# Optimization experiments

Hardware: AMD Instinct MI355X
Metric: run time of the kernel (lower is better)

The kernel has to match this reference:

```python
import jax, jax.numpy as jnp
import numpy as np

B, T, V, D = 4, 2048, 1024, 512


def setup_inputs() -> dict:
    key = jax.random.key(0)
    ks = jax.random.split(key, 6)
    x = jax.random.normal(ks[0], (B, T, V), dtype=jnp.float32)
    decay_logit = jax.random.uniform(ks[1], (), dtype=jnp.float32)
    scale = jnp.ones((), dtype=jnp.float32)
    std = 0.02
    # Linear weights stored as [in, out] so projection is x @ W
    Wq = std * jax.random.normal(ks[2], (V, D), dtype=jnp.float32)
    Wk = std * jax.random.normal(ks[3], (V, D), dtype=jnp.float32)
    Wv = std * jax.random.normal(ks[4], (V, D), dtype=jnp.float32)
    Wo = std * jax.random.normal(ks[5], (D, V), dtype=jnp.float32)
    return {"x": x, "decay_logit": decay_logit, "scale": scale,
            "Wq": Wq, "Wk": Wk, "Wv": Wv, "Wo": Wo}


def reference(x, decay_logit, scale, Wq, Wk, Wv, Wo):
    dtype = x.dtype
    xf = x.astype(jnp.float32)
    q = (xf @ Wq).astype(dtype)  # [B,T,D]
    k = (xf @ Wk).astype(dtype)
    v = (xf @ Wv).astype(dtype)
    scores = jnp.einsum('btd,bsd->bts', q, k)  # [B,T,T]
    decay = jax.nn.sigmoid(decay_logit)
    pos = jnp.arange(T)
    diff = pos[None, :] - pos[:, None]  # diff[i,j] = j - i
    expo = jnp.maximum(diff.astype(jnp.float32) - 1.0, 0.0)
    weights = (decay ** expo) * (diff > 0)  # [T,T]
    scores = scores * weights.astype(dtype)[None, :, :]
    retrieved = jnp.einsum('bts,bsd->btd', scores, v)  # [B,T,D]
    out = (retrieved.astype(jnp.float32) @ Wo).astype(dtype) * scale
    return out
```

## Files before the change

kernel.cpp:

```cpp
#include <hip/hip_runtime.h>
#include <stdint.h>


using bf16u = unsigned short;
using short8 = __attribute__((ext_vector_type(8))) short;
using f32x4  = __attribute__((ext_vector_type(4))) float;

__device__ __forceinline__ unsigned short f2bf(float f) {
  unsigned int u = __float_as_uint(f);
  u += 0x7fffu + ((u >> 16) & 1u);
  return (unsigned short)(u >> 16);
}

__device__ __forceinline__ void gload16(const void* g, void* l) {
  __builtin_amdgcn_global_load_lds(
      (const __attribute__((address_space(1))) void*)g,
      (__attribute__((address_space(3))) void*)l, 16, 0, 0);
}

#define BM 128
#define BN 128
#define BK 32

template<int MODE>
__global__ __launch_bounds__(256)
void gemm_bt(const bf16u* __restrict__ A, const bf16u* __restrict__ Bt,
             void* __restrict__ Cout,
             int K, int ldA, int ldB, int ldC,
             long sA, long sB, long sC,
             int nbx, const float* __restrict__ scal,
             const bf16u* __restrict__ vSrc, bf16u* __restrict__ vDst)
{
  __shared__ bf16u Al[2][BM * BK];
  __shared__ bf16u Bl[2][BN * BK];
  const int z = blockIdx.z;
  A  += (long)z * sA;
  Bt += (long)z * sB;

  const int tid  = threadIdx.x;
  const int orig = blockIdx.x;

  int by, bx;
  if (MODE == 1) {
    if (orig >= 32) {
      const int ti = orig - 32;
      const int c0 = (ti & 15) * 32;
      const int r0 = (ti >> 4) * 32;
      bf16u* tl = (bf16u*)&Al[0][0];
      const int tx = tid & 31, ty = tid >> 5;
      const bf16u* vin = vSrc + (long)z * (2048L * 1536);
      bf16u*      vout = vDst + (long)z * (1L << 20);
#pragma unroll
      for (int i = 0; i < 4; ++i)
        tl[(ty + 8 * i) * 33 + tx] = vin[(long)(r0 + ty + 8 * i) * 1536 + c0 + tx];
      __syncthreads();
#pragma unroll
      for (int i = 0; i < 4; ++i)
        vout[(long)(c0 + ty + 8 * i) * 2048 + r0 + tx] = tl[tx * 33 + ty + 8 * i];
      return;
    }
    by = orig >> 1; bx = orig & 1;
  } else {
    const int nwg = gridDim.x;
    const int q8 = nwg >> 3, r8 = nwg & 7;
    const int xcd = orig & 7, lid = orig >> 3;
    const int wgid = (xcd < r8 ? xcd * (q8 + 1)
                               : r8 * (q8 + 1) + (xcd - r8) * q8) + lid;
    by = wgid / nbx; bx = wgid - by * nbx;
  }
  const int bm = by * BM;
  const int bn = (MODE == 1) ? ((bm >> 7) + bx) * BN : bx * BN;
  const int kofsB = (MODE == 3) ? (bm & ~127) : 0;

  const int wid  = tid >> 6;
  const int lane = tid & 63;
  const int wr = (wid >> 1) * 64;
  const int wc = (wid & 1) * 64;

  f32x4 acc[4][4] = {};

  const int base0 = wid * 1024;
  const int lin0  = base0 + lane * 16;
  const int r0row = lin0 >> 6;
  const int r1row = r0row + 64;
  const int c16   = (lin0 >> 4) & 3;
  const int rcol  = (c16 ^ ((r0row >> 1) & 3)) << 3;

  const int nt = K / BK;

  auto stage = [&](int buf, int kk) {
    gload16(A  + (long)(bm + r0row) * ldA + kk + rcol, (char*)&Al[buf][0] + base0);
    gload16(A  + (long)(bm + r1row) * ldA + kk + rcol, (char*)&Al[buf][0] + base0 + 4096);
    gload16(Bt + (long)(bn + r0row) * ldB + kofsB + kk + rcol, (char*)&Bl[buf][0] + base0);
    gload16(Bt + (long)(bn + r1row) * ldB + kofsB + kk + rcol, (char*)&Bl[buf][0] + base0 + 4096);
  };

  stage(0, 0);
  __syncthreads();

  const int fr = lane & 15;
  const int kc = lane >> 4;
  int cur = 0;
  for (int t = 0; t < nt; ++t) {
    if (t + 1 < nt) stage(cur ^ 1, (t + 1) * BK);
    short8 af[4], bfr[4];
#pragma unroll
    for (int m = 0; m < 4; ++m) {
      int row = wr + m * 16 + fr;
      af[m] = *(const short8*)&Al[cur][row * BK + ((kc ^ ((row >> 1) & 3)) << 3)];
    }
#pragma unroll
    for (int n = 0; n < 4; ++n) {
      int row = wc + n * 16 + fr;
      bfr[n] = *(const short8*)&Bl[cur][row * BK + ((kc ^ ((row >> 1) & 3)) << 3)];
    }
#pragma unroll
    for (int m = 0; m < 4; ++m)
#pragma unroll
      for (int n = 0; n < 4; ++n)
        acc[m][n] = __builtin_amdgcn_mfma_f32_16x16x32_bf16(af[m], bfr[n], acc[m][n], 0, 0, 0);
    __syncthreads();
    cur ^= 1;
  }

  const int cc = lane & 15;
  const int cr = (lane >> 4) * 4;
  float mul = 1.0f, l2d = 0.0f;
  if (MODE == 1) {
    float dlv = scal[0];
    float decay = 1.0f / (1.0f + __expf(-dlv));
    l2d = __log2f(decay);
  } else if (MODE == 2) {
    mul = scal[0];
  }

#pragma unroll
  for (int m = 0; m < 4; ++m) {
#pragma unroll
    for (int n = 0; n < 4; ++n) {
#pragma unroll
      for (int j = 0; j < 4; ++j) {
        int row = bm + wr + m * 16 + cr + j;
        int col = bn + wc + n * 16 + cc;
        float val = acc[m][n][j];
        if (MODE == 1) {
          int diff = col - row;
          float w = (diff > 0 && col < 2048)
                        ? exp2f((float)(diff - 1) * l2d) : 0.0f;
          int lc = bx * 128 + (wc + n * 16 + cc);
          ((bf16u*)Cout)[(long)z * sC + (long)row * ldC + lc] = f2bf(val * w);
        } else if (MODE == 2) {
          ((float*)Cout)[(long)z * sC + (long)row * ldC + col] = val * mul;
        } else {
          ((bf16u*)Cout)[(long)z * sC + (long)row * ldC + col] = f2bf(val);
        }
      }
    }
  }
}

__global__ __launch_bounds__(256)
void prep(const float4* __restrict__ x, ushort4* __restrict__ x16o,
          const float* __restrict__ Wq, const float* __restrict__ Wk,
          const float* __restrict__ Wv, const float* __restrict__ Wo,
          bf16u* __restrict__ WqT, bf16u* __restrict__ WkT,
          bf16u* __restrict__ WvT, bf16u* __restrict__ WoT)
{
  __shared__ float t[32][33];
  const int bid = blockIdx.x;
  const int tid = threadIdx.x;
  if (bid < 8192) {
    int i = bid * 256 + tid;
    float4 v = x[i];
    ushort4 o;
    o.x = f2bf(v.x); o.y = f2bf(v.y); o.z = f2bf(v.z); o.w = f2bf(v.w);
    x16o[i] = o;
    return;
  }
  const int wi = bid - 8192;
  const int w  = wi >> 9;
  const int ti = wi & 511;
  const float* in; bf16u* out; int R, C;
  if (w == 0)      { in = Wq; out = WqT; R = 1024; C = 512; }
  else if (w == 1) { in = Wk; out = WkT; R = 1024; C = 512; }
  else if (w == 2) { in = Wv; out = WvT; R = 1024; C = 512; }
  else             { in = Wo; out = WoT; R = 512;  C = 1024; }
  const int nx = C >> 5;
  const int c0 = (ti % nx) * 32, r0 = (ti / nx) * 32;
  const int tx = tid & 31, ty = tid >> 5;
#pragma unroll
  for (int i = 0; i < 4; ++i)
    t[ty + 8 * i][tx] = in[(long)(r0 + ty + 8 * i) * C + c0 + tx];
  __syncthreads();
#pragma unroll
  for (int i = 0; i < 4; ++i)
    out[(long)(c0 + ty + 8 * i) * R + r0 + tx] = f2bf(t[tx][ty + 8 * i]);
}

extern "C" void kernel_launch(void* const* d_in, const int* in_sizes, int n_in,
                              void* d_out, int out_size, void* d_ws, size_t ws_size,
                              hipStream_t stream) {
  const float* x  = (const float*)d_in[0];
  const float* dl = (const float*)d_in[1];
  const float* sc = (const float*)d_in[2];
  const float* Wq = (const float*)d_in[3];
  const float* Wk = (const float*)d_in[4];
  const float* Wv = (const float*)d_in[5];
  const float* Wo = (const float*)d_in[6];

  const int B = 4, T = 2048, V = 1024, D = 512;
  const long MT = (long)B * T;
  const int QKV = 3 * D;
  const int BAND = 256;

  char* p = (char*)d_ws;
  auto alloc = [&](size_t bytes) { char* r = p; p += bytes; return r; };
  bf16u* x16 = (bf16u*)alloc((size_t)MT * V * 2);
  bf16u* WqT = (bf16u*)alloc((size_t)D * V * 2);
  bf16u* WkT = (bf16u*)alloc((size_t)D * V * 2);
  bf16u* WvT = (bf16u*)alloc((size_t)D * V * 2);
  bf16u* WoT = (bf16u*)alloc((size_t)V * D * 2);
  bf16u* qkv = (bf16u*)alloc((size_t)MT * QKV * 2);
  bf16u* vT  = (bf16u*)alloc((size_t)MT * D * 2 + 4096);
  bf16u* Sb  = (bf16u*)alloc((size_t)B * T * BAND * 2);
  bf16u* R   = (bf16u*)alloc((size_t)MT * D * 2);

  prep<<<dim3(8192 + 2048), 256, 0, stream>>>(
      (const float4*)x, (ushort4*)x16, Wq, Wk, Wv, Wo, WqT, WkT, WvT, WoT);

  gemm_bt<0><<<dim3(64 * 12, 1, 1), 256, 0, stream>>>(
      x16, WqT, qkv, V, V, V, QKV, 0, 0, 0, 12, nullptr, nullptr, nullptr);

  gemm_bt<1><<<dim3(32 + 1024, 1, B), 256, 0, stream>>>(
      qkv, qkv + D, Sb, D, QKV, QKV, BAND,
      (long)T * QKV, (long)T * QKV, (long)T * BAND, 2, dl,
      qkv + 2 * D, vT);

  gemm_bt<3><<<dim3(16 * 4, 1, B), 256, 0, stream>>>(
      Sb, vT, R, BAND, BAND, T, D,
      (long)T * BAND, (long)1 << 20, (long)T * D, 4, nullptr,
      nullptr, nullptr);

  gemm_bt<2><<<dim3(64 * 8, 1, 1), 256, 0, stream>>>(
      R, WoT, d_out, D, D, D, V, 0, 0, 0, 8, sc, nullptr, nullptr);
}
```

Measured before the change: 94.60 us.

## Reassociate (S·V)·Wo into S·(V·Wo) and drop the final projection GEMM

Computes a per-batch transposed product (V·Wo)^T inside the extra blocks of the score kernel, replacing the V transpose. The banded score GEMM then multiplies directly against this product and writes the scaled fp32 output. This removes the R intermediate, the separate output-projection launch and the transpose pass. In exchange the banded GEMM's N dimension doubles, and a larger intermediate (B×V×T bf16) is written and then re-read.

```diff
diff --git a/kernel.cpp b/kernel.cpp
--- a/kernel.cpp
+++ b/kernel.cpp
@@ -29,37 +29,35 @@
              int K, int ldA, int ldB, int ldC,
              long sA, long sB, long sC,
              int nbx, const float* __restrict__ scal,
-             const bf16u* __restrict__ vSrc, bf16u* __restrict__ vDst)
+             const bf16u* __restrict__ vSrc, const bf16u* __restrict__ wA,
+             bf16u* __restrict__ w2t)
 {
   __shared__ bf16u Al[2][BM * BK];
   __shared__ bf16u Bl[2][BN * BK];
-  const int z = blockIdx.z;
-  A  += (long)z * sA;
-  Bt += (long)z * sB;
-
+  const int z    = blockIdx.z;
   const int tid  = threadIdx.x;
   const int orig = blockIdx.x;
 
   int by, bx;
+  bool isW2 = false;
+  const bf16u* Ap;
+  const bf16u* Btp;
+  int lda = ldA, ldb = ldB;
+
   if (MODE == 1) {
     if (orig >= 32) {
-      const int ti = orig - 32;
-      const int c0 = (ti & 15) * 32;
-      const int r0 = (ti >> 4) * 32;
-      bf16u* tl = (bf16u*)&Al[0][0];
-      const int tx = tid & 31, ty = tid >> 5;
-      const bf16u* vin = vSrc + (long)z * (2048L * 1536);
-      bf16u*      vout = vDst + (long)z * (1L << 20);
-#pragma unroll
-      for (int i = 0; i < 4; ++i)
-        tl[(ty + 8 * i) * 33 + tx] = vin[(long)(r0 + ty + 8 * i) * 1536 + c0 + tx];
-      __syncthreads();
-#pragma unroll
-      for (int i = 0; i < 4; ++i)
-        vout[(long)(c0 + ty + 8 * i) * 2048 + r0 + tx] = tl[tx * 33 + ty + 8 * i];
-      return;
-    }
-    by = orig >> 1; bx = orig & 1;
+      isW2 = true;
+      const int idx = orig - 32;
+      by = idx >> 4;
+      bx = idx & 15;
+      Ap  = wA;
+      lda = 512;
+      Btp = vSrc + (long)z * sB;
+    } else {
+      by = orig >> 1; bx = orig & 1;
+      Ap  = A  + (long)z * sA;
+      Btp = Bt + (long)z * sB;
+    }
   } else {
     const int nwg = gridDim.x;
     const int q8 = nwg >> 3, r8 = nwg & 7;
@@ -67,10 +65,13 @@
     const int wgid = (xcd < r8 ? xcd * (q8 + 1)
                                : r8 * (q8 + 1) + (xcd - r8) * q8) + lid;
     by = wgid / nbx; bx = wgid - by * nbx;
-  }
+    Ap  = A  + (long)z * sA;
+    Btp = Bt + (long)z * sB;
+  }
+
   const int bm = by * BM;
-  const int bn = (MODE == 1) ? ((bm >> 7) + bx) * BN : bx * BN;
-  const int kofsB = (MODE == 3) ? (bm & ~127) : 0;
+  const int bn = (MODE == 1 && !isW2) ? ((bm >> 7) + bx) * BN : bx * BN;
+  const int kofsB = (MODE == 3) ? bm : 0;
 
   const int wid  = tid >> 6;
   const int lane = tid & 63;
@@ -89,10 +90,10 @@
   const int nt = K / BK;
 
   auto stage = [&](int buf, int kk) {
-    gload16(A  + (long)(bm + r0row) * ldA + kk + rcol, (char*)&Al[buf][0] + base0);
-    gload16(A  + (long)(bm + r1row) * ldA + kk + rcol, (char*)&Al[buf][0] + base0 + 4096);
-    gload16(Bt + (long)(bn + r0row) * ldB + kofsB + kk + rcol, (char*)&Bl[buf][0] + base0);
-    gload16(Bt + (long)(bn + r1row) * ldB + kofsB + kk + rcol, (char*)&Bl[buf][0] + base0 + 4096);
+    gload16(Ap  + (long)(bm + r0row) * lda + kk + rcol, (char*)&Al[buf][0] + base0);
+    gload16(Ap  + (long)(bm + r1row) * lda + kk + rcol, (char*)&Al[buf][0] + base0 + 4096);
+    gload16(Btp + (long)(bn + r0row) * ldb + kofsB + kk + rcol, (char*)&Bl[buf][0] + base0);
+    gload16(Btp + (long)(bn + r1row) * ldb + kofsB + kk + rcol, (char*)&Bl[buf][0] + base0 + 4096);
   };
 
   stage(0, 0);
@@ -126,11 +127,11 @@
   const int cc = lane & 15;
   const int cr = (lane >> 4) * 4;
   float mul = 1.0f, l2d = 0.0f;
-  if (MODE == 1) {
+  if (MODE == 1 && !isW2) {
     float dlv = scal[0];
     float decay = 1.0f / (1.0f + __expf(-dlv));
     l2d = __log2f(decay);
-  } else if (MODE == 2) {
+  } else if (MODE == 3) {
     mul = scal[0];
   }
 
@@ -144,12 +145,16 @@
         int col = bn + wc + n * 16 + cc;
         float val = acc[m][n][j];
         if (MODE == 1) {
-          int diff = col - row;
-          float w = (diff > 0 && col < 2048)
-                        ? exp2f((float)(diff - 1) * l2d) : 0.0f;
-          int lc = bx * 128 + (wc + n * 16 + cc);
-          ((bf16u*)Cout)[(long)z * sC + (long)row * ldC + lc] = f2bf(val * w);
-        } else if (MODE == 2) {
+          if (isW2) {
+            w2t[((long)z << 21) + ((long)row << 11) + col] = f2bf(val);
+          } else {
+            int diff = col - row;
+            float w = (diff > 0 && col < 2048)
+                          ? exp2f((float)(diff - 1) * l2d) : 0.0f;
+            int lc = bx * 128 + (wc + n * 16 + cc);
+            ((bf16u*)Cout)[(long)z * sC + (long)row * ldC + lc] = f2bf(val * w);
+          }
+        } else if (MODE == 3) {
           ((float*)Cout)[(long)z * sC + (long)row * ldC + col] = val * mul;
         } else {
           ((bf16u*)Cout)[(long)z * sC + (long)row * ldC + col] = f2bf(val);
@@ -221,26 +226,23 @@
   bf16u* WvT = (bf16u*)alloc((size_t)D * V * 2);
   bf16u* WoT = (bf16u*)alloc((size_t)V * D * 2);
   bf16u* qkv = (bf16u*)alloc((size_t)MT * QKV * 2);
-  bf16u* vT  = (bf16u*)alloc((size_t)MT * D * 2 + 4096);
   bf16u* Sb  = (bf16u*)alloc((size_t)B * T * BAND * 2);
-  bf16u* R   = (bf16u*)alloc((size_t)MT * D * 2);
+  bf16u* W2T = (bf16u*)alloc((size_t)B * V * T * 2);
 
   prep<<<dim3(8192 + 2048), 256, 0, stream>>>(
       (const float4*)x, (ushort4*)x16, Wq, Wk, Wv, Wo, WqT, WkT, WvT, WoT);
 
   gemm_bt<0><<<dim3(64 * 12, 1, 1), 256, 0, stream>>>(
-      x16, WqT, qkv, V, V, V, QKV, 0, 0, 0, 12, nullptr, nullptr, nullptr);
-
-  gemm_bt<1><<<dim3(32 + 1024, 1, B), 256, 0, stream>>>(
+      x16, WqT, qkv, V, V, V, QKV, 0, 0, 0, 12, nullptr,
+      nullptr, nullptr, nullptr);
+
+  gemm_bt<1><<<dim3(32 + 128, 1, B), 256, 0, stream>>>(
       qkv, qkv + D, Sb, D, QKV, QKV, BAND,
       (long)T * QKV, (long)T * QKV, (long)T * BAND, 2, dl,
-      qkv + 2 * D, vT);
-
-  gemm_bt<3><<<dim3(16 * 4, 1, B), 256, 0, stream>>>(
-      Sb, vT, R, BAND, BAND, T, D,
-      (long)T * BAND, (long)1 << 20, (long)T * D, 4, nullptr,
-      nullptr, nullptr);
-
-  gemm_bt<2><<<dim3(64 * 8, 1, 1), 256, 0, stream>>>(
-      R, WoT, d_out, D, D, D, V, 0, 0, 0, 8, sc, nullptr, nullptr);
-}
+      qkv + 2 * D, WoT, W2T);
+
+  gemm_bt<3><<<dim3(16 * 8, 1, B), 256, 0, stream>>>(
+      Sb, W2T, d_out, BAND, BAND, T, V,
+      (long)T * BAND, (long)V * T, (long)T * V, 8, sc,
+      nullptr, nullptr, nullptr);
+}
```

Result: faster. 83.72 us (-11.5%).
